# Optimization experiments

Hardware: AMD Instinct MI355X
Metric: run time of the kernel (lower is better)

The kernel has to match this reference:

```python
import jax, jax.numpy as jnp
import numpy as np

R = 32          # voxel grid resolution (dense occupancy)
WIN = 8         # window_size
H = 16          # num_heads
C = 1024        # channels
D = C // H      # head_dim = 64
FREQ_DIM = D // 2 // 3   # 10 (3D rope)
ROPE_BASE = 10000.0
EPS_NORM = 1e-12


def setup_inputs() -> dict:
    key = jax.random.key(0)
    ks = jax.random.split(key, 4)
    N = R * R * R
    x = jax.random.normal(ks[0], (N, C), dtype=jnp.float32)
    # dense voxel grid coords in raster (x-major) order, matching token order
    gx, gy, gz = jnp.meshgrid(jnp.arange(R), jnp.arange(R), jnp.arange(R), indexing='ij')
    coords = jnp.stack([gx.reshape(-1), gy.reshape(-1), gz.reshape(-1)], axis=-1).astype(jnp.int32)
    Wqkv = jax.random.normal(ks[1], (C, 3 * C), dtype=jnp.float32) * 0.02
    bqkv = jnp.zeros((3 * C,), dtype=jnp.float32)
    gamma_q = jnp.ones((H, D), dtype=jnp.float32)
    gamma_k = jnp.ones((H, D), dtype=jnp.float32)
    Wout = jax.random.normal(ks[2], (C, C), dtype=jnp.float32) * 0.02
    bout = jnp.zeros((C,), dtype=jnp.float32)
    return {"x": x, "coords": coords, "Wqkv": Wqkv, "bqkv": bqkv,
            "gamma_q": gamma_q, "gamma_k": gamma_k, "Wout": Wout, "bout": bout}


def _mh_rms_norm(t, gamma):
    # SparseMultiHeadRMSNorm: fp32 F.normalize(dim=-1) * gamma * sqrt(D)
    tf = t.astype(jnp.float32)
    norm = jnp.maximum(jnp.sqrt(jnp.sum(tf * tf, axis=-1, keepdims=True)), EPS_NORM)
    return ((tf / norm) * gamma * (D ** 0.5)).astype(t.dtype)


def _rope_cos_sin(coords):
    # freqs: 1.0 / 10000**(i/freq_dim), i in [0, freq_dim)
    freqs = 1.0 / ROPE_BASE ** (jnp.arange(FREQ_DIM, dtype=jnp.float32) / FREQ_DIM)
    phases = coords.astype(jnp.float32)[:, :, None] * freqs  # [N, 3, FREQ_DIM]
    phases = phases.reshape(coords.shape[0], -1)             # [N, 30]
    pad = D // 2 - phases.shape[-1]
    phases = jnp.concatenate([phases, jnp.zeros((coords.shape[0], pad), jnp.float32)], axis=-1)
    return jnp.cos(phases), jnp.sin(phases)                  # [N, D//2] each


def _apply_rope(t, cos, sin):
    # t: [N, H, D] -> pairs [N, H, D//2, 2]; complex mult by (cos + i sin)
    tp = t.reshape(t.shape[0], H, D // 2, 2)
    t0, t1 = tp[..., 0], tp[..., 1]
    c = cos[:, None, :]
    s = sin[:, None, :]
    r0 = t0 * c - t1 * s
    r1 = t0 * s + t1 * c
    return jnp.stack([r0, r1], axis=-1).reshape(t.shape).astype(t.dtype)


def _to_windows(t):
    Rw = R // WIN
    t = t.reshape(Rw, WIN, Rw, WIN, Rw, WIN, H, D)
    t = t.transpose(0, 2, 4, 1, 3, 5, 6, 7)
    return t.reshape(Rw * Rw * Rw, WIN ** 3, H, D)


def _from_windows(t):
    Rw = R // WIN
    t = t.reshape(Rw, Rw, Rw, WIN, WIN, WIN, H, D)
    t = t.transpose(0, 3, 1, 4, 2, 5, 6, 7)
    return t.reshape(R * R * R, H, D)


def reference(x, coords, Wqkv, bqkv, gamma_q, gamma_k, Wout, bout):
    N = x.shape[0]
    qkv = (x @ Wqkv + bqkv).reshape(N, 3, H, D)
    q, k, v = qkv[:, 0], qkv[:, 1], qkv[:, 2]
    # per-head QK RMSNorm (before rope, as in forward)
    q = _mh_rms_norm(q, gamma_q)
    k = _mh_rms_norm(k, gamma_k)
    # inline 3D RoPE from voxel coords
    cos, sin = _rope_cos_sin(coords)
    q = _apply_rope(q, cos, sin)
    k = _apply_rope(k, cos, sin)
    # windowed self-attention (shift_window = (0,0,0), dense grid -> exact partition)
    qw, kw, vw = _to_windows(q), _to_windows(k), _to_windows(v)
    scale = 1.0 / (D ** 0.5)
    scores = jnp.einsum('wqhd,wkhd->whqk', qw, kw) * scale   # [nw, H, T, T]
    attn = jax.nn.softmax(scores, axis=-1)
    hw = jnp.einsum('whqk,wkhd->wqhd', attn, vw)
    h = _from_windows(hw).reshape(N, C)
    return h @ Wout + bout
```

## Files before the change

### kernel.cpp

```cpp
#include <hip/hip_runtime.h>
#include <hip/hip_bf16.h>
#include <stdint.h>

#define DEV static __device__ __forceinline__

typedef __attribute__((ext_vector_type(4))) float f32x4;
typedef __attribute__((ext_vector_type(8))) short s16x8;
typedef __attribute__((ext_vector_type(4))) short s16x4;

constexpr int N_TOK = 32768;
constexpr int C_DIM = 1024;
constexpr int C3    = 3072;
constexpr int GK    = 1024;

DEV float bf2f(short u) { union { float f; uint32_t i; } x; x.i = ((uint32_t)(uint16_t)u) << 16; return x.f; }
DEV short f2bf(float f) { union { float f; uint32_t i; } x; x.f = f; uint32_t r = x.i + 0x7FFFu + ((x.i >> 16) & 1u); return (short)(r >> 16); }

DEV f32x4 mfma16(s16x8 a, s16x8 b, f32x4 c) {
  return __builtin_amdgcn_mfma_f32_16x16x32_bf16(a, b, c, 0, 0, 0);
}

DEV void gload16(const void* g, void* lds) {
  __builtin_amdgcn_global_load_lds((const __attribute__((address_space(1))) void*)g,
                                   (__attribute__((address_space(3))) void*)lds, 16, 0, 0);
}

#define SB() __builtin_amdgcn_sched_barrier(0)
#define WAIT_VM(N) do { asm volatile("s_waitcnt vmcnt(" #N ")" ::: "memory"); SB(); } while (0)
DEV void bar_top() { SB(); __builtin_amdgcn_s_barrier(); asm volatile("s_waitcnt lgkmcnt(0)" ::: "memory"); SB(); }
DEV void bar_end() { SB(); __builtin_amdgcn_s_barrier(); SB(); }

DEV float redsum16(float v) {
  v += __shfl_xor(v, 1); v += __shfl_xor(v, 2); v += __shfl_xor(v, 4); v += __shfl_xor(v, 8);
  return v;
}

__global__ void k_cvt_x(const float* __restrict__ in, short* __restrict__ outb,
                        float2* __restrict__ ctab) {
  if (blockIdx.x == 0) {
    for (int t = threadIdx.x; t < 320; t += 256) {
      int c = t / 10, fi = t % 10;
      float freq = powf(10000.0f, -(float)fi / 10.0f);
      float ph = (float)c * freq;
      ctab[t] = make_float2(cosf(ph), sinf(ph));
    }
  }
  size_t i = ((size_t)blockIdx.x * 256 + threadIdx.x) * 8;
  float4 a = *(const float4*)(in + i);
  float4 b = *(const float4*)(in + i + 4);
  s16x8 o;
  o[0] = f2bf(a.x); o[1] = f2bf(a.y); o[2] = f2bf(a.z); o[3] = f2bf(a.w);
  o[4] = f2bf(b.x); o[5] = f2bf(b.y); o[6] = f2bf(b.z); o[7] = f2bf(b.w);
  *(s16x8*)(outb + i) = o;
}

__global__ void k_transpose_all(const float* __restrict__ wqkv, short* __restrict__ wqkvT,
                                const float* __restrict__ wout, short* __restrict__ woutT) {
  __shared__ float t[32][33];
  int b = blockIdx.x;
  const float* in; short* outb; int rin, cin, bx, by;
  if (b < 96 * 32) {
    in = wqkv; outb = wqkvT; rin = C_DIM; cin = C3; bx = b % 96; by = b / 96;
  } else {
    b -= 96 * 32;
    in = wout; outb = woutT; rin = C_DIM; cin = C_DIM; bx = b % 32; by = b / 32;
  }
  int tx = threadIdx.x & 31, ty = threadIdx.x >> 5;
  int c0 = bx * 32, r0 = by * 32;
#pragma unroll
  for (int k = 0; k < 32; k += 8) t[ty + k][tx] = in[(size_t)(r0 + ty + k) * cin + c0 + tx];
  __syncthreads();
#pragma unroll
  for (int k = 0; k < 32; k += 8) outb[(size_t)(c0 + ty + k) * rin + r0 + tx] = f2bf(t[tx][ty + k]);
}

#define READ_A(b, mh) do { _Pragma("unroll") for (int mi_ = 0; mi_ < 4; ++mi_) \
  _Pragma("unroll") for (int kh_ = 0; kh_ < 2; ++kh_) af[mi_ * 2 + kh_] = LDA(b, (mh) * 4 + mi_, kh_); } while (0)
#define READ_B(b, nh, bfx) do { _Pragma("unroll") for (int ni_ = 0; ni_ < 2; ++ni_) \
  _Pragma("unroll") for (int kh_ = 0; kh_ < 2; ++kh_) (bfx)[ni_ * 2 + kh_] = LDB(b, (nh) * 2 + ni_, kh_); } while (0)
#define MFMAQ(mh, nh, bfx) do { __builtin_amdgcn_s_setprio(1); \
  _Pragma("unroll") for (int mi_ = 0; mi_ < 4; ++mi_) \
  _Pragma("unroll") for (int kh_ = 0; kh_ < 2; ++kh_) \
  _Pragma("unroll") for (int ni_ = 0; ni_ < 2; ++ni_) \
    acc[(mh) * 4 + mi_][(nh) * 2 + ni_] = mfma16(af[mi_ * 2 + kh_], (bfx)[ni_ * 2 + kh_], acc[(mh) * 4 + mi_][(nh) * 2 + ni_]); \
  __builtin_amdgcn_s_setprio(0); } while (0)

DEV void gemm256_core(const short* __restrict__ A, const short* __restrict__ Bt,
                      int tileM, int tileN, short* lds, f32x4 (&acc)[8][4]) {
  const int tid = threadIdx.x;
  const int lane = tid & 63, wid = tid >> 6;
  const int wr = wid >> 2, wc = wid & 3;
  const int g = lane >> 4, r = lane & 15;

#pragma unroll
  for (int mi = 0; mi < 8; ++mi)
#pragma unroll
    for (int ni = 0; ni < 4; ++ni) acc[mi][ni] = (f32x4)0.0f;

  const short* Ag = A + (size_t)tileM * GK;
  const short* Bg = Bt + (size_t)tileN * GK;
  const int ldsA = wr * 8192;
  const int ldsB = 16384 + (wc >> 1) * 8192;
  const int brow = (wc & 1) * 64;

  auto stageA = [&](int b, int h, int kt) {
    const short* gb = Ag + (size_t)(h * 128) * GK + kt * 64;
    short* db = lds + b * 32768 + h * 8192 + (tid & 448) * 8;
#pragma unroll
    for (int i = 0; i < 2; ++i) {
      int s = i * 512 + tid;
      int row = s >> 3;
      int c = (s & 7) ^ (row & 7);
      gload16(gb + (size_t)row * GK + c * 8, db + i * 4096);
    }
  };
  auto stageB = [&](int b, int h, int kt) {
    const short* gb = Bg + (size_t)(h * 128) * GK + kt * 64;
    short* db = lds + b * 32768 + 16384 + h * 8192 + (tid & 448) * 8;
#pragma unroll
    for (int i = 0; i < 2; ++i) {
      int s = i * 512 + tid;
      int row = s >> 3;
      int c = (s & 7) ^ (row & 7);
      gload16(gb + (size_t)row * GK + c * 8, db + i * 4096);
    }
  };
  auto LDA = [&](int b, int mi, int kh) -> s16x8 {
    int row = mi * 16 + r;
    int c = (kh * 4 + g) ^ (r & 7);
    return *(const s16x8*)(lds + b * 32768 + ldsA + row * 64 + c * 8);
  };
  auto LDB = [&](int b, int ni, int kh) -> s16x8 {
    int row = brow + ni * 16 + r;
    int c = (kh * 4 + g) ^ (r & 7);
    return *(const s16x8*)(lds + b * 32768 + ldsB + row * 64 + c * 8);
  };

  s16x8 af[8], bf0[4], bf1[4];

  stageA(0, 0, 0); stageA(0, 1, 0); stageB(0, 0, 0); stageB(0, 1, 0);
  stageB(1, 0, 1); stageB(1, 1, 1);
  WAIT_VM(4);
  __builtin_amdgcn_s_barrier();

#pragma unroll 1
  for (int t = 0; t < 16; t += 2) {
    const bool s2 = (t + 2 < 16), s3 = (t + 3 < 16);
    READ_A(0, 0); READ_B(0, 0, bf0);
    stageA(1, 0, t + 1);
    bar_top(); MFMAQ(0, 0, bf0); bar_end();
    READ_B(0, 1, bf1);
    stageA(1, 1, t + 1);
    bar_top(); MFMAQ(0, 1, bf1); bar_end();
    READ_A(0, 1);
    if (s2) stageB(0, 0, t + 2);
    bar_top(); MFMAQ(1, 0, bf0); bar_end();
    if (s2) stageB(0, 1, t + 2);
    bar_top(); MFMAQ(1, 1, bf1);
    if (s2) { WAIT_VM(4); } else { WAIT_VM(0); }
    bar_end();
    READ_A(1, 0); READ_B(1, 0, bf0);
    if (s2) stageA(0, 0, t + 2);
    bar_top(); MFMAQ(0, 0, bf0); bar_end();
    READ_B(1, 1, bf1);
    if (s2) stageA(0, 1, t + 2);
    bar_top(); MFMAQ(0, 1, bf1); bar_end();
    READ_A(1, 1);
    if (s3) stageB(1, 0, t + 3);
    bar_top(); MFMAQ(1, 0, bf0); bar_end();
    if (s3) stageB(1, 1, t + 3);
    bar_top(); MFMAQ(1, 1, bf1);
    WAIT_VM(4);
    bar_end();
  }
}

__global__ __launch_bounds__(512, 2) void k_gemm_qkv(const short* __restrict__ A, const short* __restrict__ Bt,
                                                     const float* __restrict__ bias,
                                                     const float* __restrict__ gq, const float* __restrict__ gk,
                                                     const float2* __restrict__ ctab,
                                                     short* __restrict__ qw, short* __restrict__ kw,
                                                     short* __restrict__ vw) {
  __shared__ __align__(16) short lds[65536];
  const int nwg = gridDim.x, q8 = nwg >> 3, bid = blockIdx.x;
  const int sb = (bid & 7) * q8 + (bid >> 3);
  const int bx = sb % 12, by = sb / 12;
  const int tileM = by * 256, tileN = bx * 256;
  f32x4 acc[8][4];
  gemm256_core(A, Bt, tileM, tileN, lds, acc);

  const int tid = threadIdx.x, lane = tid & 63, wid = tid >> 6;
  const int wr = wid >> 2, wc = wid & 3, g = lane >> 4, r = lane & 15;
  const int colbase = tileN + wc * 64;
  const int part = colbase >> 10;
  const int head = (colbase >> 6) & 15;
  if (part < 2) {
    __syncthreads();
    float2* ctl = (float2*)lds;
    if (tid < 320) ctl[tid] = ctab[tid];
    __syncthreads();
    short* buf = (part == 0) ? qw : kw;
    const float* gamma = (part == 0) ? gq : gk;
    const float qk_sc = (part == 0) ? 1.4426950408889634f : 8.0f;
    float gam[4];
#pragma unroll
    for (int ni = 0; ni < 4; ++ni) gam[ni] = gamma[head * 64 + ni * 16 + r];
#pragma unroll
    for (int mi = 0; mi < 8; ++mi) {
#pragma unroll
      for (int j = 0; j < 4; ++j) {
        int gr = tileM + wr * 128 + mi * 16 + g * 4 + j;
        int gx = gr >> 10, gy = (gr >> 5) & 31, gz = gr & 31;
        int w = ((gx >> 3) << 4) | ((gy >> 3) << 2) | (gz >> 3);
        int idx = ((gx & 7) << 6) | ((gy & 7) << 3) | (gz & 7);
        size_t base = ((size_t)(w * 16 + head) * 512 + idx) * 64;
        float v[4];
        float ss = 0.f;
#pragma unroll
        for (int ni = 0; ni < 4; ++ni) {
          v[ni] = acc[mi][ni][j] + bias[colbase + ni * 16 + r];
          ss += v[ni] * v[ni];
        }
        ss = redsum16(ss);
        float sc = qk_sc / fmaxf(sqrtf(ss), 1e-12f);
#pragma unroll
        for (int ni = 0; ni < 4; ++ni) v[ni] *= sc * gam[ni];
#pragma unroll
        for (int ni = 0; ni < 4; ++ni) {
          int p = ni * 8 + (r >> 1);
          float c = 1.f, s = 0.f;
          if (p < 30) {
            int axis = (p >= 20) ? 2 : (p >= 10 ? 1 : 0);
            int fi = p - axis * 10;
            int cc = (axis == 0) ? gx : ((axis == 1) ? gy : gz);
            float2 cs = ctl[cc * 10 + fi];
            c = cs.x; s = cs.y;
          }
          float vp = __shfl_xor(v[ni], 1);
          float res = (r & 1) ? (vp * s + v[ni] * c) : (v[ni] * c - vp * s);
          buf[base + ni * 16 + r] = f2bf(res);
        }
      }
    }
  } else {
#pragma unroll
    for (int mi = 0; mi < 8; ++mi) {
#pragma unroll
      for (int j = 0; j < 4; ++j) {
        int gr = tileM + wr * 128 + mi * 16 + g * 4 + j;
        int gx = gr >> 10, gy = (gr >> 5) & 31, gz = gr & 31;
        int w = ((gx >> 3) << 4) | ((gy >> 3) << 2) | (gz >> 3);
        int idx = ((gx & 7) << 6) | ((gy & 7) << 3) | (gz & 7);
        size_t base = (size_t)(w * 16 + head) * 32768 + idx;
#pragma unroll
        for (int ni = 0; ni < 4; ++ni) {
          int d = ni * 16 + r;
          vw[base + (size_t)d * 512] = f2bf(acc[mi][ni][j] + bias[colbase + d]);
        }
      }
    }
  }
}

__global__ __launch_bounds__(512, 2) void k_gemm_out(const short* __restrict__ A, const short* __restrict__ Bt,
                                                     const float* __restrict__ bias, float* __restrict__ out) {
  __shared__ __align__(16) short lds[65536];
  const int nwg = gridDim.x, q8 = nwg >> 3, bid = blockIdx.x;
  const int sb = (bid & 7) * q8 + (bid >> 3);
  const int bx = sb & 3, by = sb >> 2;
  const int tileM = by * 256, tileN = bx * 256;
  f32x4 acc[8][4];
  gemm256_core(A, Bt, tileM, tileN, lds, acc);

  const int tid = threadIdx.x, lane = tid & 63, wid = tid >> 6;
  const int wr = wid >> 2, wc = wid & 3, g = lane >> 4, r = lane & 15;
#pragma unroll
  for (int mi = 0; mi < 8; ++mi)
#pragma unroll
    for (int j = 0; j < 4; ++j) {
      int gr = tileM + wr * 128 + mi * 16 + g * 4 + j;
#pragma unroll
      for (int ni = 0; ni < 4; ++ni) {
        int gc = tileN + wc * 64 + ni * 16 + r;
        out[(size_t)gr * C_DIM + gc] = acc[mi][ni][j] + bias[gc];
      }
    }
}

__global__ __launch_bounds__(256, 2) void k_attn(const short* __restrict__ qw, const short* __restrict__ kw,
                                                 const short* __restrict__ vw, short* __restrict__ hb) {
  __shared__ __align__(16) short Ks[2][4096];
  __shared__ __align__(16) short Vt[2][4096];
  __shared__ __align__(16) short Pb[4][1024];
  const int b = blockIdx.x;
  const int qh = b & 1, head = (b >> 1) & 15, w = b >> 5;
  const int tid = threadIdx.x, lane = tid & 63, wid = tid >> 6;
  const int g = lane >> 4, r = lane & 15;
  const short* Qp = qw + ((size_t)(w * 16 + head) * 512 + qh * 256 + wid * 64) * 64;
  const short* Kp = kw + (size_t)(w * 16 + head) * 32768;
  const short* Vp = vw + (size_t)(w * 16 + head) * 32768;

  s16x8 qf[4][2];
#pragma unroll
  for (int qt = 0; qt < 4; ++qt)
#pragma unroll
    for (int kh = 0; kh < 2; ++kh)
      qf[qt][kh] = *(const s16x8*)(Qp + (qt * 16 + r) * 64 + kh * 32 + g * 8);

  f32x4 o[4][4];
#pragma unroll
  for (int qt = 0; qt < 4; ++qt)
#pragma unroll
    for (int nt = 0; nt < 4; ++nt) o[qt][nt] = (f32x4)0.f;
  float m[4] = {-1e30f, -1e30f, -1e30f, -1e30f};
  float l[4] = {0.f, 0.f, 0.f, 0.f};

  short* PwW = &Pb[wid][0];

  auto stageK = [&](int bufb, int c) {
#pragma unroll
    for (int i = 0; i < 2; ++i) {
      int ci = i * 256 + tid;
      int row = ci >> 3;
      int sc = (ci & 7) ^ (row & 7);
      gload16(Kp + (size_t)(c * 64 + row) * 64 + sc * 8, &Ks[bufb][(i * 256 + (tid & ~63)) * 8]);
    }
  };
  auto stageV = [&](int bufb, int c) {
#pragma unroll
    for (int i = 0; i < 2; ++i) {
      int ci = i * 256 + tid;
      int row = ci >> 3;
      int sc = (ci & 7) ^ (row & 7);
      gload16(Vp + (size_t)row * 512 + c * 64 + sc * 8, &Vt[bufb][(i * 256 + (tid & ~63)) * 8]);
    }
  };

  stageK(0, 0); stageV(0, 0);

#pragma unroll 1
  for (int c = 0; c < 8; ++c) {
    const int cur = c & 1;
    if (c < 7) { stageK(cur ^ 1, c + 1); stageV(cur ^ 1, c + 1); }
    if (c < 7) { WAIT_VM(4); } else { WAIT_VM(0); }
    __builtin_amdgcn_s_barrier();

    s16x8 kf[4][2];
#pragma unroll
    for (int nt = 0; nt < 4; ++nt)
#pragma unroll
      for (int kh = 0; kh < 2; ++kh)
        kf[nt][kh] = *(const s16x8*)(&Ks[cur][0] + (nt * 16 + r) * 64 + (((kh * 4 + g) ^ (r & 7)) << 3));
    s16x8 vfr[4][2];
#pragma unroll
    for (int nt = 0; nt < 4; ++nt)
#pragma unroll
      for (int kh = 0; kh < 2; ++kh)
        vfr[nt][kh] = *(const s16x8*)(&Vt[cur][0] + (nt * 16 + r) * 64 + (((kh * 4 + g) ^ (r & 7)) << 3));

#pragma unroll
    for (int qt = 0; qt < 4; ++qt) {
      f32x4 s4[4];
#pragma unroll
      for (int nt = 0; nt < 4; ++nt) s4[nt] = (f32x4)0.f;
      __builtin_amdgcn_s_setprio(1);
#pragma unroll
      for (int nt = 0; nt < 4; ++nt)
#pragma unroll
        for (int kh = 0; kh < 2; ++kh) s4[nt] = mfma16(kf[nt][kh], qf[qt][kh], s4[nt]);
      __builtin_amdgcn_s_setprio(0);
      float pm = -1e30f;
#pragma unroll
      for (int nt = 0; nt < 4; ++nt)
#pragma unroll
        for (int j = 0; j < 4; ++j) pm = fmaxf(pm, s4[nt][j]);
      pm = fmaxf(pm, __shfl_xor(pm, 16));
      pm = fmaxf(pm, __shfl_xor(pm, 32));
      float mn = fmaxf(m[qt], pm);
      float al = exp2f(m[qt] - mn);
      m[qt] = mn;
      float ps = 0.f;
#pragma unroll
      for (int nt = 0; nt < 4; ++nt)
#pragma unroll
        for (int j = 0; j < 4; ++j) { float p = exp2f(s4[nt][j] - mn); s4[nt][j] = p; ps += p; }
      ps += __shfl_xor(ps, 16);
      ps += __shfl_xor(ps, 32);
      l[qt] = l[qt] * al + ps;
#pragma unroll
      for (int nt = 0; nt < 4; ++nt) o[qt][nt] *= al;
#pragma unroll
      for (int nt = 0; nt < 4; ++nt) {
        uint32_t u0 = (uint32_t)(uint16_t)f2bf(s4[nt][0]) | ((uint32_t)(uint16_t)f2bf(s4[nt][1]) << 16);
        uint32_t u1 = (uint32_t)(uint16_t)f2bf(s4[nt][2]) | ((uint32_t)(uint16_t)f2bf(s4[nt][3]) << 16);
        int col = nt * 16 + g * 4;
        int slot = (col >> 3) ^ (r & 7);
        uint2 uu; uu.x = u0; uu.y = u1;
        *(uint2*)(PwW + r * 64 + slot * 8 + (g & 1) * 4) = uu;
      }
      s16x8 pf0 = *(const s16x8*)(PwW + r * 64 + ((g ^ (r & 7)) << 3));
      s16x8 pf1 = *(const s16x8*)(PwW + r * 64 + (((4 + g) ^ (r & 7)) << 3));
      __builtin_amdgcn_s_setprio(1);
#pragma unroll
      for (int nt = 0; nt < 4; ++nt) {
        o[qt][nt] = mfma16(vfr[nt][0], pf0, o[qt][nt]);
        o[qt][nt] = mfma16(vfr[nt][1], pf1, o[qt][nt]);
      }
      __builtin_amdgcn_s_setprio(0);
    }
    asm volatile("s_waitcnt lgkmcnt(0)" ::: "memory");
    SB();
    __builtin_amdgcn_s_barrier();
  }

#pragma unroll
  for (int qt = 0; qt < 4; ++qt) {
    float inv = 1.f / l[qt];
#pragma unroll
    for (int nt = 0; nt < 4; ++nt) {
      uint32_t u0 = (uint32_t)(uint16_t)f2bf(o[qt][nt][0] * inv) | ((uint32_t)(uint16_t)f2bf(o[qt][nt][1] * inv) << 16);
      uint32_t u1 = (uint32_t)(uint16_t)f2bf(o[qt][nt][2] * inv) | ((uint32_t)(uint16_t)f2bf(o[qt][nt][3] * inv) << 16);
      int col = nt * 16 + g * 4;
      int slot = (col >> 3) ^ (r & 7);
      uint2 uu; uu.x = u0; uu.y = u1;
      *(uint2*)(PwW + r * 64 + slot * 8 + (g & 1) * 4) = uu;
    }
#pragma unroll
    for (int rr = 0; rr < 2; ++rr) {
      int q2 = lane >> 2;
      int cc = (lane & 3) + rr * 4;
      int slot = cc ^ (q2 & 7);
      s16x8 vv = *(const s16x8*)(PwW + q2 * 64 + slot * 8);
      int idx = qh * 256 + wid * 64 + qt * 16 + q2;
      int cx = ((w >> 4) << 3) + (idx >> 6);
      int cy = (((w >> 2) & 3) << 3) + ((idx >> 3) & 7);
      int cz = ((w & 3) << 3) + (idx & 7);
      size_t n = (size_t)cx * 1024 + cy * 32 + cz;
      *(s16x8*)(hb + n * 1024 + head * 64 + cc * 8) = vv;
    }
  }
}

extern "C" void kernel_launch(void* const* d_in, const int* in_sizes, int n_in,
                              void* d_out, int out_size, void* d_ws, size_t ws_size,
                              hipStream_t stream) {
  const float* x    = (const float*)d_in[0];
  const float* Wqkv = (const float*)d_in[2];
  const float* bqkv = (const float*)d_in[3];
  const float* gq   = (const float*)d_in[4];
  const float* gk   = (const float*)d_in[5];
  const float* Wout = (const float*)d_in[6];
  const float* bout = (const float*)d_in[7];
  float* out = (float*)d_out;

  char* ws = (char*)d_ws;
  size_t o = 0;
  auto take = [&](size_t b) { char* p = ws + o; o += (b + 255) & ~(size_t)255; return p; };
  short* xb    = (short*)take((size_t)N_TOK * C_DIM * 2);
  short* wqkvT = (short*)take((size_t)C3 * C_DIM * 2);
  short* woutT = (short*)take((size_t)C_DIM * C_DIM * 2);
  float2* ctab = (float2*)take(320 * sizeof(float2));
  short* qw    = (short*)take((size_t)N_TOK * C_DIM * 2);
  short* kw    = (short*)take((size_t)N_TOK * C_DIM * 2);
  short* vw    = (short*)take((size_t)N_TOK * C_DIM * 2);
  short* hb = xb;

  k_cvt_x<<<(N_TOK * C_DIM) / (256 * 8), 256, 0, stream>>>(x, xb, ctab);
  k_transpose_all<<<96 * 32 + 32 * 32, 256, 0, stream>>>(Wqkv, wqkvT, Wout, woutT);
  k_gemm_qkv<<<(C3 / 256) * (N_TOK / 256), 512, 0, stream>>>(xb, wqkvT, bqkv, gq, gk, ctab, qw, kw, vw);
  k_attn<<<2048, 256, 0, stream>>>(qw, kw, vw, hb);
  k_gemm_out<<<(C_DIM / 256) * (N_TOK / 256), 512, 0, stream>>>(hb, woutT, bout, out);
}
```

Before: 514.9 us.

## Compute QKV GEMM transposed so epilogue writes head-dim contiguous vectors

Swaps the GEMM operands so the QKV projection produces W^T·X^T: tile rows now index output channels and tile columns index tokens. Each lane then holds four consecutive head-dim values, so the q/k epilogue can do the RoPE pair rotation in registers, reduce the RMS norm with two cross-group shuffles, and write 8-byte vector stores instead of scattered 2-byte stores. The aim is cheaper, more coalesced epilogue writes and fewer shuffles. The V path still does strided scalar stores, and the changed tile traversal alters cache reuse of the operands.

Result: no change. 515.8 us (+0.2%).

```diff
diff --git a/kernel.cpp b/kernel.cpp
--- a/kernel.cpp
+++ b/kernel.cpp
@@ -29,11 +29,6 @@
 #define WAIT_VM(N) do { asm volatile("s_waitcnt vmcnt(" #N ")" ::: "memory"); SB(); } while (0)
 DEV void bar_top() { SB(); __builtin_amdgcn_s_barrier(); asm volatile("s_waitcnt lgkmcnt(0)" ::: "memory"); SB(); }
 DEV void bar_end() { SB(); __builtin_amdgcn_s_barrier(); SB(); }
-
-DEV float redsum16(float v) {
-  v += __shfl_xor(v, 1); v += __shfl_xor(v, 2); v += __shfl_xor(v, 4); v += __shfl_xor(v, 8);
-  return v;
-}
 
 __global__ void k_cvt_x(const float* __restrict__ in, short* __restrict__ outb,
                         float2* __restrict__ ctab) {
@@ -184,16 +179,27 @@
   __shared__ __align__(16) short lds[65536];
   const int nwg = gridDim.x, q8 = nwg >> 3, bid = blockIdx.x;
   const int sb = (bid & 7) * q8 + (bid >> 3);
-  const int bx = sb % 12, by = sb / 12;
+  const int bx = sb % 128, by = sb / 128;
   const int tileM = by * 256, tileN = bx * 256;
   f32x4 acc[8][4];
   gemm256_core(A, Bt, tileM, tileN, lds, acc);
 
   const int tid = threadIdx.x, lane = tid & 63, wid = tid >> 6;
   const int wr = wid >> 2, wc = wid & 3, g = lane >> 4, r = lane & 15;
-  const int colbase = tileN + wc * 64;
-  const int part = colbase >> 10;
-  const int head = (colbase >> 6) & 15;
+  const int part = tileM >> 10;
+  const int rowabs = tileM + wr * 128;
+  const int rowloc = rowabs & 1023;
+
+  int tw[4], tidx[4], tcx[4], tcy[4], tcz[4];
+#pragma unroll
+  for (int ni = 0; ni < 4; ++ni) {
+    int tok = tileN + wc * 64 + ni * 16 + r;
+    int gx = tok >> 10, gy = (tok >> 5) & 31, gz = tok & 31;
+    tw[ni] = ((gx >> 3) << 4) | ((gy >> 3) << 2) | (gz >> 3);
+    tidx[ni] = ((gx & 7) << 6) | ((gy & 7) << 3) | (gz & 7);
+    tcx[ni] = gx; tcy[ni] = gy; tcz[ni] = gz;
+  }
+
   if (part < 2) {
     __syncthreads();
     float2* ctl = (float2*)lds;
@@ -202,61 +208,81 @@
     short* buf = (part == 0) ? qw : kw;
     const float* gamma = (part == 0) ? gq : gk;
     const float qk_sc = (part == 0) ? 1.4426950408889634f : 8.0f;
-    float gam[4];
-#pragma unroll
-    for (int ni = 0; ni < 4; ++ni) gam[ni] = gamma[head * 64 + ni * 16 + r];
-#pragma unroll
-    for (int mi = 0; mi < 8; ++mi) {
-#pragma unroll
-      for (int j = 0; j < 4; ++j) {
-        int gr = tileM + wr * 128 + mi * 16 + g * 4 + j;
-        int gx = gr >> 10, gy = (gr >> 5) & 31, gz = gr & 31;
-        int w = ((gx >> 3) << 4) | ((gy >> 3) << 2) | (gz >> 3);
-        int idx = ((gx & 7) << 6) | ((gy & 7) << 3) | (gz & 7);
-        size_t base = ((size_t)(w * 16 + head) * 512 + idx) * 64;
-        float v[4];
+#pragma unroll
+    for (int hh = 0; hh < 2; ++hh) {
+      const int head = (rowloc >> 6) + hh;
+      float gam[4][4], bv[4][4];
+#pragma unroll
+      for (int mh = 0; mh < 4; ++mh)
+#pragma unroll
+        for (int j = 0; j < 4; ++j) {
+          int d = mh * 16 + g * 4 + j;
+          gam[mh][j] = gamma[head * 64 + d];
+          bv[mh][j] = bias[rowabs + hh * 64 + mh * 16 + g * 4 + j];
+        }
+#pragma unroll
+      for (int ni = 0; ni < 4; ++ni) {
+        float vv[4][4];
         float ss = 0.f;
 #pragma unroll
-        for (int ni = 0; ni < 4; ++ni) {
-          v[ni] = acc[mi][ni][j] + bias[colbase + ni * 16 + r];
-          ss += v[ni] * v[ni];
-        }
-        ss = redsum16(ss);
+        for (int mh = 0; mh < 4; ++mh)
+#pragma unroll
+          for (int j = 0; j < 4; ++j) {
+            vv[mh][j] = acc[hh * 4 + mh][ni][j] + bv[mh][j];
+            ss += vv[mh][j] * vv[mh][j];
+          }
+        ss += __shfl_xor(ss, 16);
+        ss += __shfl_xor(ss, 32);
         float sc = qk_sc / fmaxf(sqrtf(ss), 1e-12f);
 #pragma unroll
-        for (int ni = 0; ni < 4; ++ni) v[ni] *= sc * gam[ni];
-#pragma unroll
-        for (int ni = 0; ni < 4; ++ni) {
-          int p = ni * 8 + (r >> 1);
-          float c = 1.f, s = 0.f;
-          if (p < 30) {
-            int axis = (p >= 20) ? 2 : (p >= 10 ? 1 : 0);
-            int fi = p - axis * 10;
-            int cc = (axis == 0) ? gx : ((axis == 1) ? gy : gz);
-            float2 cs = ctl[cc * 10 + fi];
-            c = cs.x; s = cs.y;
+        for (int mh = 0; mh < 4; ++mh)
+#pragma unroll
+          for (int j = 0; j < 4; ++j) vv[mh][j] *= sc * gam[mh][j];
+#pragma unroll
+        for (int mh = 0; mh < 4; ++mh)
+#pragma unroll
+          for (int pp = 0; pp < 2; ++pp) {
+            int p = mh * 8 + g * 2 + pp;
+            if (p < 30) {
+              int axis = (p >= 20) ? 2 : (p >= 10 ? 1 : 0);
+              int fi = p - axis * 10;
+              int cc = (axis == 0) ? tcx[ni] : ((axis == 1) ? tcy[ni] : tcz[ni]);
+              float2 cs = ctl[cc * 10 + fi];
+              float t0 = vv[mh][2 * pp], t1 = vv[mh][2 * pp + 1];
+              vv[mh][2 * pp]     = t0 * cs.x - t1 * cs.y;
+              vv[mh][2 * pp + 1] = t0 * cs.y + t1 * cs.x;
+            }
           }
-          float vp = __shfl_xor(v[ni], 1);
-          float res = (r & 1) ? (vp * s + v[ni] * c) : (v[ni] * c - vp * s);
-          buf[base + ni * 16 + r] = f2bf(res);
+        size_t base = ((size_t)(tw[ni] * 16 + head) * 512 + tidx[ni]) * 64;
+#pragma unroll
+        for (int mh = 0; mh < 4; ++mh) {
+          s16x4 o4;
+#pragma unroll
+          for (int j = 0; j < 4; ++j) o4[j] = f2bf(vv[mh][j]);
+          *(s16x4*)(buf + base + mh * 16 + g * 4) = o4;
         }
       }
     }
   } else {
 #pragma unroll
-    for (int mi = 0; mi < 8; ++mi) {
-#pragma unroll
-      for (int j = 0; j < 4; ++j) {
-        int gr = tileM + wr * 128 + mi * 16 + g * 4 + j;
-        int gx = gr >> 10, gy = (gr >> 5) & 31, gz = gr & 31;
-        int w = ((gx >> 3) << 4) | ((gy >> 3) << 2) | (gz >> 3);
-        int idx = ((gx & 7) << 6) | ((gy & 7) << 3) | (gz & 7);
-        size_t base = (size_t)(w * 16 + head) * 32768 + idx;
-#pragma unroll
-        for (int ni = 0; ni < 4; ++ni) {
-          int d = ni * 16 + r;
-          vw[base + (size_t)d * 512] = f2bf(acc[mi][ni][j] + bias[colbase + d]);
-        }
+    for (int hh = 0; hh < 2; ++hh) {
+      const int head = (rowloc >> 6) + hh;
+      float bv[4][4];
+#pragma unroll
+      for (int mh = 0; mh < 4; ++mh)
+#pragma unroll
+        for (int j = 0; j < 4; ++j)
+          bv[mh][j] = bias[rowabs + hh * 64 + mh * 16 + g * 4 + j];
+#pragma unroll
+      for (int ni = 0; ni < 4; ++ni) {
+        size_t wb = (size_t)(tw[ni] * 16 + head) * 32768 + tidx[ni];
+#pragma unroll
+        for (int mh = 0; mh < 4; ++mh)
+#pragma unroll
+          for (int j = 0; j < 4; ++j) {
+            int d = mh * 16 + g * 4 + j;
+            vw[wb + (size_t)d * 512] = f2bf(acc[hh * 4 + mh][ni][j] + bv[mh][j]);
+          }
       }
     }
   }
@@ -467,7 +493,7 @@
 
   k_cvt_x<<<(N_TOK * C_DIM) / (256 * 8), 256, 0, stream>>>(x, xb, ctab);
   k_transpose_all<<<96 * 32 + 32 * 32, 256, 0, stream>>>(Wqkv, wqkvT, Wout, woutT);
-  k_gemm_qkv<<<(C3 / 256) * (N_TOK / 256), 512, 0, stream>>>(xb, wqkvT, bqkv, gq, gk, ctab, qw, kw, vw);
+  k_gemm_qkv<<<(C3 / 256) * (N_TOK / 256), 512, 0, stream>>>(wqkvT, xb, bqkv, gq, gk, ctab, qw, kw, vw);
   k_attn<<<2048, 256, 0, stream>>>(qw, kw, vw, hb);
   k_gemm_out<<<(C_DIM / 256) * (N_TOK / 256), 512, 0, stream>>>(hb, woutT, bout, out);
 }
```
